# Performance work log

Measured on AMD Instinct MI355X. Metric: run time of the kernel, lower is better.

## Reference

```python
import jax, jax.numpy as jnp
import numpy as np

B, N, K, C = 4, 4096, 32, 192  # batch, npoint, nsample, channels (C % 6 == 0)
EPS = 1e-5


def setup_inputs() -> dict:
    key = jax.random.key(0)
    ks = jax.random.split(key, 8)
    p = jax.random.normal(ks[0], (B, N, 3), jnp.float32)
    x = jax.random.normal(ks[1], (B, C, N), jnp.float32)
    idx = jax.random.randint(ks[2], (B, N, K), 0, N)  # ball-query neighbor ids
    W = jax.random.normal(ks[3], (C, C + 3), jnp.float32) * 0.05  # 1x1 conv weight
    gamma = 1.0 + 0.1 * jax.random.normal(ks[4], (C,), jnp.float32)
    beta = 0.1 * jax.random.normal(ks[5], (C,), jnp.float32)
    rmean = 0.1 * jax.random.normal(ks[6], (C,), jnp.float32)
    rvar = jax.random.uniform(ks[7], (C,), jnp.float32) + 0.5  # positive running var
    return dict(p=p, x=x, idx=idx, W=W, gamma=gamma, beta=beta, rmean=rmean, rvar=rvar)


def reference(p, x, idx, W, gamma, beta, rmean, rvar):
    # --- grouper: gather neighbors, relative coords ---
    pn = jax.vmap(lambda pp, ii: pp[ii])(p, idx)            # [B,N,K,3]
    dp = jnp.transpose(pn - p[:, :, None, :], (0, 3, 1, 2))  # [B,3,N,K]
    xj = jax.vmap(lambda xx, ii: xx[:, ii])(x, idx)          # [B,C,N,K]
    # --- PosPool sin/cos positional embedding fused with features ---
    feat_dim = C // 6
    dim_mat = jnp.power(500.0, jnp.arange(feat_dim, dtype=jnp.float32) / feat_dim)
    div = (50.0 * dp)[..., None] / dim_mat                   # [B,3,N,K,fd]
    pe = jnp.concatenate([jnp.sin(div), jnp.cos(div)], axis=-1)  # [B,3,N,K,2fd]
    pe = jnp.transpose(pe, (0, 1, 4, 2, 3)).reshape(B, C, N, K)  # [B,C,N,K]
    agg = xj * pe + pe
    # --- dp_fj concat -> 1x1 conv -> BN(eval) -> ReLU ---
    h = jnp.concatenate([dp, agg], axis=1)                   # [B,C+3,N,K]
    y = jnp.einsum('oc,bcnk->bonk', W, h)                    # [B,C,N,K]
    inv = gamma / jnp.sqrt(rvar + EPS)
    y = y * inv[:, None, None] + (beta - rmean * inv)[:, None, None]
    y = jax.nn.relu(y)
    # --- max reduction over neighbors ---
    return jnp.max(y, axis=-1)                               # [B,C,N]
```

## Files before the change

### kernel.cpp

```cpp
#include <hip/hip_runtime.h>
#include <math.h>

#define B_   4
#define N_   4096
#define K_   32
#define C_   192
#define CH_  195
#define KPAD 224
#define PTS  2
#define NKT  7
#define NNT  4
#define GRID ((B_ * N_) / PTS)

using half8  = __attribute__((ext_vector_type(8))) _Float16;
using half2v = __attribute__((ext_vector_type(2))) _Float16;
using f32x4  = __attribute__((ext_vector_type(4))) float;

__device__ _Float16 g_Wp[C_ * KPAD];
__device__ _Float16 g_xT[(size_t)B_ * N_ * C_];

__device__ __forceinline__ float dpp_max16(float v) {
    int s;
    s = __builtin_amdgcn_update_dpp(0, __float_as_int(v), 0xB1,  0xF, 0xF, true);
    v = fmaxf(v, __int_as_float(s));
    s = __builtin_amdgcn_update_dpp(0, __float_as_int(v), 0x4E,  0xF, 0xF, true);
    v = fmaxf(v, __int_as_float(s));
    s = __builtin_amdgcn_update_dpp(0, __float_as_int(v), 0x141, 0xF, 0xF, true);
    v = fmaxf(v, __int_as_float(s));
    s = __builtin_amdgcn_update_dpp(0, __float_as_int(v), 0x140, 0xF, 0xF, true);
    v = fmaxf(v, __int_as_float(s));
    return v;
}

__global__ __launch_bounds__(256) void prep(const float* __restrict__ x,
                                            const float* __restrict__ W,
                                            const float* __restrict__ gamma_,
                                            const float* __restrict__ rvar) {
    __shared__ float s[32][97];
    const int tid = threadIdx.x;
    if (blockIdx.x < 1024) {
        const int bi = blockIdx.x;
        const int b  = bi >> 8;
        const int c0 = ((bi >> 7) & 1) * 96;
        const int n0 = (bi & 127) * 32;
#pragma unroll
        for (int it = 0; it < 3; ++it) {
            const int c  = it * 32 + (tid >> 3);
            const int n4 = (tid & 7) * 4;
            const float4 v = *(const float4*)(x + ((size_t)b * C_ + c0 + c) * N_ + n0 + n4);
            s[n4 + 0][c] = v.x; s[n4 + 1][c] = v.y; s[n4 + 2][c] = v.z; s[n4 + 3][c] = v.w;
        }
        __syncthreads();
#pragma unroll
        for (int it = 0; it < 2; ++it) {
            const int t = it * 256 + tid;
            if (t < 32 * 12) {
                const int n  = t / 12;
                const int ch = t - n * 12;
                half8 v;
#pragma unroll
                for (int jj = 0; jj < 8; ++jj) v[jj] = (_Float16)s[n][ch * 8 + jj];
                *(half8*)(g_xT + ((size_t)b * N_ + n0 + n) * C_ + c0 + ch * 8) = v;
            }
        }
    } else {
        const int i = (blockIdx.x - 1024) * 256 + tid;
        if (i < C_ * KPAD) {
            const int o = i / KPAD, r = i - o * KPAD;
            const float inv = gamma_[o] * rsqrtf(rvar[o] + 1e-5f);
            float v = 0.0f;
            if (r < 3)                  v = W[o * CH_ + r];
            else if (r >= 8 && r < 200) v = W[o * CH_ + 3 + (r - 8)];
            g_Wp[i] = (_Float16)(v * inv);
        }
    }
}

__global__ __launch_bounds__(256, 5) void la_mfma(
    const float* __restrict__ p,
    const int*   __restrict__ idx,
    const float* __restrict__ gamma_,
    const float* __restrict__ beta_,
    const float* __restrict__ rmean,
    const float* __restrict__ rvar,
    float* __restrict__ out)
{
    __shared__ _Float16 hb[NKT * NNT * 64 * 8];
    __shared__ float s_bias[C_], s_fr[32], s_out[C_ * PTS];

    const int tid  = threadIdx.x;
    const int lane = tid & 63;
    const int w    = tid >> 6;
    const int l15  = lane & 15;
    const int quad = lane >> 4;

    const int q  = blockIdx.x & 7;
    const int sI = blockIdx.x >> 3;
    const int L  = q * (GRID / 8) + sI;
    const int bn0 = L * PTS;
    const int b   = bn0 >> 12;
    const int n0  = bn0 & (N_ - 1);

    if (tid < C_) {
        const float inv = gamma_[tid] * rsqrtf(rvar[tid] + 1e-5f);
        s_bias[tid] = beta_[tid] - rmean[tid] * inv;
    }
    if (tid < 32) s_fr[tid] = 7.9577471546f * exp2f(-(float)tid * 0.2801808715263400f);
    __syncthreads();

    {
        const int col = w * 16 + l15;
        const int pt  = col >> 5;
        const int k   = col & 31;
        const int gp  = bn0 + pt;
        const int j   = idx[(size_t)gp * K_ + k];
        const float d0 = p[(size_t)(b * N_ + j) * 3 + 0] - p[(size_t)gp * 3 + 0];
        const float d1 = p[(size_t)(b * N_ + j) * 3 + 1] - p[(size_t)gp * 3 + 1];
        const float d2 = p[(size_t)(b * N_ + j) * 3 + 2] - p[(size_t)gp * 3 + 2];
        const _Float16* xh = g_xT + ((size_t)b * N_ + j) * C_;

        float sfr[8];
#pragma unroll
        for (int jj = 0; jj < 8; ++jj) sfr[jj] = s_fr[quad * 8 + jj];

#pragma unroll
        for (int i6 = 0; i6 < 6; ++i6) {
            const int chunk = quad + 4 * i6;
            const half8 v = *(const half8*)(xh + chunk * 8);
            const float dd  = (chunk < 8) ? d0 : ((chunk < 16) ? d1 : d2);
            const float off = (chunk & 4) ? 0.25f : 0.0f;
            half8 hv;
#pragma unroll
            for (int jj = 0; jj < 8; jj += 2) {
                const float pe0 = __builtin_amdgcn_sinf(fmaf(dd, sfr[jj],     off));
                const float pe1 = __builtin_amdgcn_sinf(fmaf(dd, sfr[jj + 1], off));
                const half2v pe2 = __builtin_bit_cast(half2v, __builtin_amdgcn_cvt_pkrtz(pe0, pe1));
                half2v v2; v2[0] = v[jj]; v2[1] = v[jj + 1];
                const half2v r2 = pe2 * v2 + pe2;
                hv[jj] = r2[0]; hv[jj + 1] = r2[1];
            }
            const int ro = chunk + 1;
            const int kt = ro >> 2, kq = ro & 3;
            *(half8*)(&hb[(size_t)((kt * NNT + w) * 64 + kq * 16 + l15) * 8]) = hv;
        }
        if (quad == 0) {
            half8 hv0 = (half8)(_Float16)0.0f;
            hv0[0] = (_Float16)d0; hv0[1] = (_Float16)d1; hv0[2] = (_Float16)d2;
            *(half8*)(&hb[(size_t)((0 * NNT + w) * 64 + 0 * 16 + l15) * 8]) = hv0;
        } else {
            const int ro = 24 + quad;
            const int kt = ro >> 2, kq = ro & 3;
            *(half8*)(&hb[(size_t)((kt * NNT + w) * 64 + kq * 16 + l15) * 8]) = (half8)(_Float16)0.0f;
        }
    }
    __syncthreads();

    f32x4 acc[3][4];
#pragma unroll
    for (int i = 0; i < 3; ++i)
#pragma unroll
        for (int t = 0; t < 4; ++t) acc[i][t] = (f32x4)0.0f;

#pragma unroll
    for (int kt = 0; kt < NKT; ++kt) {
        const int k0 = kt * 32 + quad * 8;
        half8 a[3], bf[4];
#pragma unroll
        for (int i = 0; i < 3; ++i) {
            const int m = (w * 3 + i) * 16 + l15;
            a[i] = *(const half8*)(g_Wp + (size_t)m * KPAD + k0);
        }
#pragma unroll
        for (int t = 0; t < 4; ++t)
            bf[t] = *(const half8*)(&hb[(size_t)((kt * NNT + t) * 64 + lane) * 8]);
#pragma unroll
        for (int i = 0; i < 3; ++i)
#pragma unroll
            for (int t = 0; t < 4; ++t)
                acc[i][t] = __builtin_amdgcn_mfma_f32_16x16x32_f16(a[i], bf[t], acc[i][t], 0, 0, 0);
    }

#pragma unroll
    for (int i = 0; i < 3; ++i) {
        const int mbase = (w * 3 + i) * 16 + quad * 4;
#pragma unroll
        for (int pt = 0; pt < PTS; ++pt) {
            const f32x4 va = acc[i][2 * pt];
            const f32x4 vb = acc[i][2 * pt + 1];
#pragma unroll
            for (int r = 0; r < 4; ++r) {
                float v = fmaxf(va[r], vb[r]);
                v = dpp_max16(v);
                if (l15 == 0) {
                    const int m = mbase + r;
                    s_out[m * PTS + pt] = fmaxf(v + s_bias[m], 0.0f);
                }
            }
        }
    }
    __syncthreads();

    if (tid < C_) {
        const float2 o2 = *(const float2*)(&s_out[tid * PTS]);
        *(float2*)(&out[((size_t)b * C_ + tid) * N_ + n0]) = o2;
    }
}

extern "C" void kernel_launch(void* const* d_in, const int* in_sizes, int n_in,
                              void* d_out, int out_size, void* d_ws, size_t ws_size,
                              hipStream_t stream) {
    (void)in_sizes; (void)n_in; (void)out_size; (void)d_ws; (void)ws_size;
    const float* p      = (const float*)d_in[0];
    const float* x      = (const float*)d_in[1];
    const int*   idx    = (const int*)d_in[2];
    const float* W      = (const float*)d_in[3];
    const float* gamma_ = (const float*)d_in[4];
    const float* beta_  = (const float*)d_in[5];
    const float* rmean  = (const float*)d_in[6];
    const float* rvar   = (const float*)d_in[7];
    float* out = (float*)d_out;

    prep<<<1024 + (C_ * KPAD + 255) / 256, 256, 0, stream>>>(x, W, gamma_, rvar);
    la_mfma<<<GRID, 256, 0, stream>>>(p, idx, gamma_, beta_, rmean, rvar, out);
}
```

Measured before the change: 169.9 us.

## Make MFMA kernel persistent over 8 point groups with prefetch of next gather

The main kernel now runs 1024 blocks, and each block loops over 8 consecutive two-point groups instead of launching one block per group. While the MFMA loop for the current group runs, it loads the next group's neighbor index, coordinates and fp16 features into registers, so gather latency overlaps with compute. Per-block setup of bias and frequencies is paid once per 8 groups. The occupancy hint drops from 5 to 4 blocks per SM to make room for the extra registers. The prep kernel also reads shared memory as float4 with a padded row stride.

```diff
diff --git a/kernel.cpp b/kernel.cpp
--- a/kernel.cpp
+++ b/kernel.cpp
@@ -10,7 +10,8 @@
 #define PTS  2
 #define NKT  7
 #define NNT  4
-#define GRID ((B_ * N_) / PTS)
+#define G_   8
+#define GRID 1024
 
 using half8  = __attribute__((ext_vector_type(8))) _Float16;
 using half2v = __attribute__((ext_vector_type(2))) _Float16;
@@ -36,7 +37,7 @@
                                             const float* __restrict__ W,
                                             const float* __restrict__ gamma_,
                                             const float* __restrict__ rvar) {
-    __shared__ float s[32][97];
+    __shared__ float s[32][100];
     const int tid = threadIdx.x;
     if (blockIdx.x < 1024) {
         const int bi = blockIdx.x;
@@ -57,9 +58,13 @@
             if (t < 32 * 12) {
                 const int n  = t / 12;
                 const int ch = t - n * 12;
+                const float4 f0 = *(const float4*)(&s[n][ch * 8 + 0]);
+                const float4 f1 = *(const float4*)(&s[n][ch * 8 + 4]);
                 half8 v;
-#pragma unroll
-                for (int jj = 0; jj < 8; ++jj) v[jj] = (_Float16)s[n][ch * 8 + jj];
+                v[0] = (_Float16)f0.x; v[1] = (_Float16)f0.y;
+                v[2] = (_Float16)f0.z; v[3] = (_Float16)f0.w;
+                v[4] = (_Float16)f1.x; v[5] = (_Float16)f1.y;
+                v[6] = (_Float16)f1.z; v[7] = (_Float16)f1.w;
                 *(half8*)(g_xT + ((size_t)b * N_ + n0 + n) * C_ + c0 + ch * 8) = v;
             }
         }
@@ -76,7 +81,7 @@
     }
 }
 
-__global__ __launch_bounds__(256, 5) void la_mfma(
+__global__ __launch_bounds__(256, 4) void la_mfma(
     const float* __restrict__ p,
     const int*   __restrict__ idx,
     const float* __restrict__ gamma_,
@@ -94,12 +99,9 @@
     const int l15  = lane & 15;
     const int quad = lane >> 4;
 
-    const int q  = blockIdx.x & 7;
-    const int sI = blockIdx.x >> 3;
-    const int L  = q * (GRID / 8) + sI;
-    const int bn0 = L * PTS;
-    const int b   = bn0 >> 12;
-    const int n0  = bn0 & (N_ - 1);
+    const int q    = blockIdx.x & 7;
+    const int li   = blockIdx.x >> 3;
+    const int grp0 = (q * 128 + li) * G_;
 
     if (tid < C_) {
         const float inv = gamma_[tid] * rsqrtf(rvar[tid] + 1e-5f);
@@ -108,101 +110,137 @@
     if (tid < 32) s_fr[tid] = 7.9577471546f * exp2f(-(float)tid * 0.2801808715263400f);
     __syncthreads();
 
+    float sfr[8];
+#pragma unroll
+    for (int jj = 0; jj < 8; ++jj) sfr[jj] = s_fr[quad * 8 + jj];
+
+    const int colB = w * 16 + l15;
+    const int ptB  = colB >> 5;
+    const int kB   = colB & 31;
+
+    int   bn0 = grp0 * PTS;
+    int   b   = bn0 >> 12;
+    int   n0  = bn0 & (N_ - 1);
+    float d0, d1, d2;
+    half8 xv[6];
     {
-        const int col = w * 16 + l15;
-        const int pt  = col >> 5;
-        const int k   = col & 31;
-        const int gp  = bn0 + pt;
-        const int j   = idx[(size_t)gp * K_ + k];
-        const float d0 = p[(size_t)(b * N_ + j) * 3 + 0] - p[(size_t)gp * 3 + 0];
-        const float d1 = p[(size_t)(b * N_ + j) * 3 + 1] - p[(size_t)gp * 3 + 1];
-        const float d2 = p[(size_t)(b * N_ + j) * 3 + 2] - p[(size_t)gp * 3 + 2];
+        const int gp = bn0 + ptB;
+        const int j  = idx[(size_t)gp * K_ + kB];
+        const float* pj = p + (size_t)(b * N_ + j) * 3;
+        const float* pn = p + (size_t)gp * 3;
+        d0 = pj[0] - pn[0]; d1 = pj[1] - pn[1]; d2 = pj[2] - pn[2];
         const _Float16* xh = g_xT + ((size_t)b * N_ + j) * C_;
-
-        float sfr[8];
-#pragma unroll
-        for (int jj = 0; jj < 8; ++jj) sfr[jj] = s_fr[quad * 8 + jj];
-
-#pragma unroll
-        for (int i6 = 0; i6 < 6; ++i6) {
-            const int chunk = quad + 4 * i6;
-            const half8 v = *(const half8*)(xh + chunk * 8);
-            const float dd  = (chunk < 8) ? d0 : ((chunk < 16) ? d1 : d2);
-            const float off = (chunk & 4) ? 0.25f : 0.0f;
-            half8 hv;
-#pragma unroll
-            for (int jj = 0; jj < 8; jj += 2) {
-                const float pe0 = __builtin_amdgcn_sinf(fmaf(dd, sfr[jj],     off));
-                const float pe1 = __builtin_amdgcn_sinf(fmaf(dd, sfr[jj + 1], off));
-                const half2v pe2 = __builtin_bit_cast(half2v, __builtin_amdgcn_cvt_pkrtz(pe0, pe1));
-                half2v v2; v2[0] = v[jj]; v2[1] = v[jj + 1];
-                const half2v r2 = pe2 * v2 + pe2;
-                hv[jj] = r2[0]; hv[jj + 1] = r2[1];
-            }
-            const int ro = chunk + 1;
-            const int kt = ro >> 2, kq = ro & 3;
-            *(half8*)(&hb[(size_t)((kt * NNT + w) * 64 + kq * 16 + l15) * 8]) = hv;
-        }
-        if (quad == 0) {
-            half8 hv0 = (half8)(_Float16)0.0f;
-            hv0[0] = (_Float16)d0; hv0[1] = (_Float16)d1; hv0[2] = (_Float16)d2;
-            *(half8*)(&hb[(size_t)((0 * NNT + w) * 64 + 0 * 16 + l15) * 8]) = hv0;
-        } else {
-            const int ro = 24 + quad;
-            const int kt = ro >> 2, kq = ro & 3;
-            *(half8*)(&hb[(size_t)((kt * NNT + w) * 64 + kq * 16 + l15) * 8]) = (half8)(_Float16)0.0f;
-        }
-    }
-    __syncthreads();
-
-    f32x4 acc[3][4];
-#pragma unroll
-    for (int i = 0; i < 3; ++i)
-#pragma unroll
-        for (int t = 0; t < 4; ++t) acc[i][t] = (f32x4)0.0f;
-
-#pragma unroll
-    for (int kt = 0; kt < NKT; ++kt) {
-        const int k0 = kt * 32 + quad * 8;
-        half8 a[3], bf[4];
+#pragma unroll
+        for (int i = 0; i < 6; ++i) xv[i] = *(const half8*)(xh + (quad + 4 * i) * 8);
+    }
+
+    for (int g = 0; g < G_; ++g) {
+        {
+#pragma unroll
+            for (int i6 = 0; i6 < 6; ++i6) {
+                const int chunk = quad + 4 * i6;
+                const half8 v = xv[i6];
+                const float dd  = (chunk < 8) ? d0 : ((chunk < 16) ? d1 : d2);
+                const float off = (chunk & 4) ? 0.25f : 0.0f;
+                half8 hv;
+#pragma unroll
+                for (int jj = 0; jj < 8; jj += 2) {
+                    const float pe0 = __builtin_amdgcn_sinf(fmaf(dd, sfr[jj],     off));
+                    const float pe1 = __builtin_amdgcn_sinf(fmaf(dd, sfr[jj + 1], off));
+                    const half2v pe2 = __builtin_bit_cast(half2v, __builtin_amdgcn_cvt_pkrtz(pe0, pe1));
+                    half2v v2; v2[0] = v[jj]; v2[1] = v[jj + 1];
+                    const half2v r2 = pe2 * v2 + pe2;
+                    hv[jj] = r2[0]; hv[jj + 1] = r2[1];
+                }
+                const int ro = chunk + 1;
+                const int kt = ro >> 2, kq = ro & 3;
+                *(half8*)(&hb[(size_t)((kt * NNT + w) * 64 + kq * 16 + l15) * 8]) = hv;
+            }
+            if (quad == 0) {
+                half8 hv0 = (half8)(_Float16)0.0f;
+                hv0[0] = (_Float16)d0; hv0[1] = (_Float16)d1; hv0[2] = (_Float16)d2;
+                *(half8*)(&hb[(size_t)((0 * NNT + w) * 64 + 0 * 16 + l15) * 8]) = hv0;
+            } else {
+                const int ro = 24 + quad;
+                const int kt = ro >> 2, kq = ro & 3;
+                *(half8*)(&hb[(size_t)((kt * NNT + w) * 64 + kq * 16 + l15) * 8]) = (half8)(_Float16)0.0f;
+            }
+        }
+        __syncthreads();
+
+        const bool has = (g + 1 < G_);
+        int j_nx = 0, bn0n = 0, bn = 0, gpn = 0;
+        if (has) {
+            bn0n = (grp0 + g + 1) * PTS;
+            bn   = bn0n >> 12;
+            gpn  = bn0n + ptB;
+            j_nx = idx[(size_t)gpn * K_ + kB];
+        }
+
+        f32x4 acc[3][4];
+#pragma unroll
+        for (int i = 0; i < 3; ++i)
+#pragma unroll
+            for (int t = 0; t < 4; ++t) acc[i][t] = (f32x4)0.0f;
+
+#pragma unroll
+        for (int kt = 0; kt < NKT; ++kt) {
+            const int k0 = kt * 32 + quad * 8;
+            half8 a[3], bf[4];
+#pragma unroll
+            for (int i = 0; i < 3; ++i) {
+                const int m = (w * 3 + i) * 16 + l15;
+                a[i] = *(const half8*)(g_Wp + (size_t)m * KPAD + k0);
+            }
+#pragma unroll
+            for (int t = 0; t < 4; ++t)
+                bf[t] = *(const half8*)(&hb[(size_t)((kt * NNT + t) * 64 + lane) * 8]);
+#pragma unroll
+            for (int i = 0; i < 3; ++i)
+#pragma unroll
+                for (int t = 0; t < 4; ++t)
+                    acc[i][t] = __builtin_amdgcn_mfma_f32_16x16x32_f16(a[i], bf[t], acc[i][t], 0, 0, 0);
+        }
+
+        float nd0 = 0.0f, nd1 = 0.0f, nd2 = 0.0f;
+        if (has) {
+            const float* pj = p + (size_t)(bn * N_ + j_nx) * 3;
+            const float* pn = p + (size_t)gpn * 3;
+            nd0 = pj[0] - pn[0]; nd1 = pj[1] - pn[1]; nd2 = pj[2] - pn[2];
+            const _Float16* xh = g_xT + ((size_t)bn * N_ + j_nx) * C_;
+#pragma unroll
+            for (int i = 0; i < 6; ++i) xv[i] = *(const half8*)(xh + (quad + 4 * i) * 8);
+        }
+
 #pragma unroll
         for (int i = 0; i < 3; ++i) {
-            const int m = (w * 3 + i) * 16 + l15;
-            a[i] = *(const half8*)(g_Wp + (size_t)m * KPAD + k0);
-        }
-#pragma unroll
-        for (int t = 0; t < 4; ++t)
-            bf[t] = *(const half8*)(&hb[(size_t)((kt * NNT + t) * 64 + lane) * 8]);
-#pragma unroll
-        for (int i = 0; i < 3; ++i)
-#pragma unroll
-            for (int t = 0; t < 4; ++t)
-                acc[i][t] = __builtin_amdgcn_mfma_f32_16x16x32_f16(a[i], bf[t], acc[i][t], 0, 0, 0);
-    }
-
-#pragma unroll
-    for (int i = 0; i < 3; ++i) {
-        const int mbase = (w * 3 + i) * 16 + quad * 4;
-#pragma unroll
-        for (int pt = 0; pt < PTS; ++pt) {
-            const f32x4 va = acc[i][2 * pt];
-            const f32x4 vb = acc[i][2 * pt + 1];
-#pragma unroll
-            for (int r = 0; r < 4; ++r) {
-                float v = fmaxf(va[r], vb[r]);
-                v = dpp_max16(v);
-                if (l15 == 0) {
-                    const int m = mbase + r;
-                    s_out[m * PTS + pt] = fmaxf(v + s_bias[m], 0.0f);
+            const int mbase = (w * 3 + i) * 16 + quad * 4;
+#pragma unroll
+            for (int pt = 0; pt < PTS; ++pt) {
+                const f32x4 va = acc[i][2 * pt];
+                const f32x4 vb = acc[i][2 * pt + 1];
+#pragma unroll
+                for (int r = 0; r < 4; ++r) {
+                    float v = fmaxf(va[r], vb[r]);
+                    v = dpp_max16(v);
+                    if (l15 == 0) {
+                        const int m = mbase + r;
+                        s_out[m * PTS + pt] = fmaxf(v + s_bias[m], 0.0f);
+                    }
                 }
             }
         }
-    }
-    __syncthreads();
-
-    if (tid < C_) {
-        const float2 o2 = *(const float2*)(&s_out[tid * PTS]);
-        *(float2*)(&out[((size_t)b * C_ + tid) * N_ + n0]) = o2;
+        __syncthreads();
+
+        if (tid < C_) {
+            const float2 o2 = *(const float2*)(&s_out[tid * PTS]);
+            *(float2*)(&out[((size_t)b * C_ + tid) * N_ + n0]) = o2;
+        }
+
+        if (has) {
+            d0 = nd0; d1 = nd1; d2 = nd2;
+            bn0 = bn0n; b = bn; n0 = bn0n & (N_ - 1);
+        }
     }
 }
 
```

Measured after the change: 276.2 us. +62.5%, slower.
